# Kernel optimization log

Measured on AMD Instinct MI355X. Metric: run time of the kernel, lower is better.

## Reference

```python
import jax, jax.numpy as jnp
import numpy as np

V = 8000      # vocab size
D = 300       # node hidden size (GloVe-300)
B = 128       # documents per batch
L = 300       # max_length
NGRAM = 3     # window radius -> K = 2*NGRAM+1 neighbors (incl. self)
T = 2         # message-passing steps
E_NUM = 2_000_000  # edges_num (edge-weight embedding rows)
C = 54        # class_num


def setup_inputs() -> dict:
    key = jax.random.key(0)
    ks = jax.random.split(key, 6)
    docs = jax.random.randint(ks[0], (B, L), 0, V)                       # token ids per doc
    node_embed = jax.random.normal(ks[1], (V, D), jnp.float32) * 0.1     # node_hidden.weight
    node_eta = jax.random.uniform(ks[2], (V, 1), jnp.float32)            # node_eta.weight (rand init)
    edge_w = jax.random.uniform(ks[3], (E_NUM, 1), jnp.float32)          # seq_edge_w.weight (rand init)
    edges_matrix = jax.random.randint(ks[4], (V, V), 0, E_NUM, dtype=jnp.int32)  # word-pair -> edge id
    bn_gamma = jnp.ones((D,), jnp.float32)
    bn_beta = jnp.zeros((D,), jnp.float32)
    W = jax.random.normal(ks[5], (D, C), jnp.float32) * 0.05             # Linear weight
    b = jnp.zeros((C,), jnp.float32)
    return {"node_embed": node_embed, "node_eta": node_eta, "edge_w": edge_w,
            "bn_gamma": bn_gamma, "bn_beta": bn_beta, "W": W, "b": b,
            "docs": docs, "edges_matrix": edges_matrix}


def reference(node_embed, node_eta, edge_w, bn_gamma, bn_beta, W, b, docs, edges_matrix):
    B_, L_ = docs.shape
    # sliding-window graph (direction == 'both'): each position connects to +/-NGRAM positions
    offs = jnp.arange(-NGRAM, NGRAM + 1)                 # [K]
    nbr = jnp.arange(L_)[:, None] + offs[None, :]        # [L, K]
    valid = (nbr >= 0) & (nbr < L_)                      # mask edges off the doc ends
    nbrc = jnp.clip(nbr, 0, L_ - 1)

    src_words = docs[:, nbrc]                            # [B, L, K] neighbor token ids
    eids = edges_matrix[docs[:, :, None], src_words]     # [B, L, K] PMI edge-id gather
    w = edge_w[eids, 0]                                  # [B, L, K] edge weights

    h = node_embed[docs]                                 # [B, L, D] node features
    eta = node_eta[docs]                                 # [B, L, 1] per-word gate
    neg = jnp.finfo(h.dtype).min

    for _ in range(T):  # fixed small T: structural loop, not a data-dim loop
        nbr_h = h[:, nbrc, :]                            # [B, L, K, D]
        msg = jnp.max(jnp.where(valid[None, :, :, None], w[..., None] * nbr_h, neg), axis=2)
        h = eta * h + (1.0 - eta) * msg                  # gated update

    pooled = jnp.sum(h, axis=1)                          # [B, D] graph readout
    x = jax.nn.relu(pooled)
    mean = x.mean(axis=0)                                # BatchNorm1d (training-mode batch stats)
    var = x.var(axis=0)
    x = (x - mean) / jnp.sqrt(var + 1e-5) * bn_gamma + bn_beta
    return jax.nn.sigmoid(x @ W + b)                     # [B, C] multi-label probs
```

## Files before the change

kernel.cpp:

```cpp
#include <hip/hip_runtime.h>
#include <hip/hip_bf16.h>
#include <math.h>

#define V     8000
#define D_    300
#define B_    128
#define L_    300
#define C_    54
#define CHUNK 10
#define STR   11
#define NELEM (L_ * CHUNK)
#define KPT   12

__global__ __launch_bounds__(256) void wgather_kernel(
    const float* __restrict__ edge_w,
    const float* __restrict__ node_eta,
    const int*   __restrict__ docs,
    const int*   __restrict__ edges_matrix,
    float* __restrict__ w_ws,
    float* __restrict__ eta_ws)
{
    int idx = blockIdx.x * 256 + threadIdx.x;
    if (idx >= B_ * L_ * 7) return;
    int b   = idx / (L_ * 7);
    int rem = idx - b * (L_ * 7);
    int l   = rem / 7;
    int o   = rem - l * 7;
    const int* drow = docs + b * L_;
    int d1 = drow[l];
    int nb = min(max(l + o - 3, 0), L_ - 1);
    int d2 = drow[nb];
    int eid = edges_matrix[(size_t)d1 * V + d2];
    w_ws[((size_t)b * L_ + l) * 8 + o] = edge_w[eid];
    if (o == 3) eta_ws[b * L_ + l] = node_eta[d1];
}

__global__ __launch_bounds__(256, 4) void prop_kernel(
    const float* __restrict__ node_embed,
    const float* __restrict__ eta_ws,
    const float* __restrict__ w_ws,
    const int*   __restrict__ docs,
    float* __restrict__ pooled)
{
    int b   = blockIdx.y;
    int d0  = blockIdx.x * CHUNK;
    int tid = threadIdx.x;

    __shared__ float h_s[L_ * STR];
    __shared__ float w_s[L_ * 8];
    __shared__ float eta_s[L_];
    __shared__ int   docs_s[L_];
    __shared__ float red[25 * CHUNK];

    for (int l = tid; l < L_; l += 256) {
        docs_s[l] = docs[b * L_ + l];
        eta_s[l]  = eta_ws[b * L_ + l];
    }
    for (int i = tid; i < L_ * 8; i += 256)
        w_s[i] = w_ws[(size_t)b * (L_ * 8) + i];
    __syncthreads();

    #pragma unroll
    for (int k = 0; k < KPT; ++k) {
        int e = tid + k * 256;
        if (e < NELEM) {
            int l  = e / CHUNK;
            int dd = e - l * CHUNK;
            h_s[l * STR + dd] = node_embed[(size_t)docs_s[l] * D_ + d0 + dd];
        }
    }
    __syncthreads();

    for (int step = 0; step < 2; ++step) {
        float nv[KPT];
        #pragma unroll
        for (int k = 0; k < KPT; ++k) {
            int e = tid + k * 256;
            if (e < NELEM) {
                int l  = e / CHUNK;
                int dd = e - l * CHUNK;
                int a  = l * STR + dd;
                float own = h_s[a];
                float msg = -3.402823466e38f;
                #pragma unroll
                for (int o = 0; o < 7; ++o) {
                    int nb = l + o - 3;
                    if ((unsigned)nb < (unsigned)L_) {
                        float hv = (o == 3) ? own : h_s[a + (o - 3) * STR];
                        msg = fmaxf(msg, w_s[l * 8 + o] * hv);
                    }
                }
                float et = eta_s[l];
                nv[k] = et * own + (1.f - et) * msg;
            }
        }
        __syncthreads();
        #pragma unroll
        for (int k = 0; k < KPT; ++k) {
            int e = tid + k * 256;
            if (e < NELEM) {
                int l  = e / CHUNK;
                int dd = e - l * CHUNK;
                h_s[l * STR + dd] = nv[k];
            }
        }
        __syncthreads();
    }

    int grp = tid / CHUNK;
    int dd  = tid - grp * CHUNK;
    if (grp < 25) {
        float s = 0.f;
        #pragma unroll
        for (int j = 0; j < 12; ++j)
            s += h_s[(grp + j * 25) * STR + dd];
        red[grp * CHUNK + dd] = s;
    }
    __syncthreads();
    if (tid < CHUNK) {
        float s = 0.f;
        #pragma unroll
        for (int g = 0; g < 25; ++g) s += red[g * CHUNK + tid];
        pooled[b * D_ + d0 + tid] = s;
    }
}

__global__ __launch_bounds__(128) void bn_kernel(
    const float* __restrict__ pooled,
    const float* __restrict__ gamma,
    const float* __restrict__ beta,
    float* __restrict__ xn)
{
    int d = blockIdx.x;
    int b = threadIdx.x;
    float x = fmaxf(pooled[b * D_ + d], 0.f);

    float v1 = x, v2 = x * x;
    #pragma unroll
    for (int off = 32; off > 0; off >>= 1) {
        v1 += __shfl_down(v1, off, 64);
        v2 += __shfl_down(v2, off, 64);
    }
    __shared__ float s1[2], s2[2];
    int lane = b & 63, wv = b >> 6;
    if (lane == 0) { s1[wv] = v1; s2[wv] = v2; }
    __syncthreads();
    float mean = (s1[0] + s1[1]) * (1.f / 128.f);
    float var  = (s2[0] + s2[1]) * (1.f / 128.f) - mean * mean;
    float xh = (x - mean) / sqrtf(var + 1e-5f);
    xn[b * D_ + d] = xh * gamma[d] + beta[d];
}

__global__ __launch_bounds__(64) void out_kernel(
    const float* __restrict__ xn,
    const float* __restrict__ Wm,
    const float* __restrict__ bias,
    float* __restrict__ out)
{
    int b = blockIdx.x;
    int c = threadIdx.x;
    if (c >= C_) return;
    float acc = bias[c];
    for (int k = 0; k < D_; ++k)
        acc = fmaf(xn[b * D_ + k], Wm[k * C_ + c], acc);
    out[b * C_ + c] = 1.f / (1.f + expf(-acc));
}

extern "C" void kernel_launch(void* const* d_in, const int* in_sizes, int n_in,
                              void* d_out, int out_size, void* d_ws, size_t ws_size,
                              hipStream_t stream) {
    const float* node_embed   = (const float*)d_in[0];
    const float* node_eta     = (const float*)d_in[1];
    const float* edge_w       = (const float*)d_in[2];
    const float* bn_gamma     = (const float*)d_in[3];
    const float* bn_beta      = (const float*)d_in[4];
    const float* Wm           = (const float*)d_in[5];
    const float* bias         = (const float*)d_in[6];
    const int*   docs         = (const int*)d_in[7];
    const int*   edges_matrix = (const int*)d_in[8];
    float* out = (float*)d_out;

    float* w_ws   = (float*)d_ws;
    float* eta_ws = w_ws + (size_t)B_ * L_ * 8;
    float* pooled = eta_ws + (size_t)B_ * L_;
    float* xn     = pooled + (size_t)B_ * D_;

    {
        int total = B_ * L_ * 7;
        wgather_kernel<<<(total + 255) / 256, 256, 0, stream>>>(
            edge_w, node_eta, docs, edges_matrix, w_ws, eta_ws);
    }
    {
        dim3 grid(D_ / CHUNK, B_);
        prop_kernel<<<grid, 256, 0, stream>>>(node_embed, eta_ws, w_ws, docs, pooled);
    }
    bn_kernel<<<D_, 128, 0, stream>>>(pooled, bn_gamma, bn_beta, xn);
    out_kernel<<<B_, 64, 0, stream>>>(xn, Wm, bias, out);
}
```

Measured before the change: 381.6 us.

## Register-tile propagation with sliding windows, double-buffered LDS, and register-held weights

Each thread now owns one feature column over a run of 12 consecutive positions. It loads an 18-element sliding window from shared memory once per step instead of 7 reads per element, and keeps edge weights and eta in registers loaded with float4 reads. Ping-pong h buffers remove the extra barrier and writeback phase per step, and the docs/weights staging through shared memory is dropped. In exchange, register pressure rises sharply (about 96 weights plus a window), only 250 of 256 threads do work, and the occupancy hint in the launch bounds is removed.

After: 389.5 us. +2.1%, slower.

```diff
diff --git a/kernel.cpp b/kernel.cpp
--- a/kernel.cpp
+++ b/kernel.cpp
@@ -10,7 +10,8 @@
 #define CHUNK 10
 #define STR   11
 #define NELEM (L_ * CHUNK)
-#define KPT   12
+#define LRUN  12
+#define NGRP  25
 
 __global__ __launch_bounds__(256) void wgather_kernel(
     const float* __restrict__ edge_w,
@@ -35,7 +36,52 @@
     if (o == 3) eta_ws[b * L_ + l] = node_eta[d1];
 }
 
-__global__ __launch_bounds__(256, 4) void prop_kernel(
+__device__ __forceinline__ void prop_step(
+    const float* __restrict__ src, float* __restrict__ dst,
+    int l0, int dd, int lg, bool active,
+    const float w[LRUN][8], const float eta[LRUN])
+{
+    float win[18];
+    #pragma unroll
+    for (int i = 0; i < 18; ++i) {
+        int l = min(max(l0 - 3 + i, 0), L_ - 1);
+        win[i] = src[l * STR + dd];
+    }
+    if (active) {
+        if (lg > 0 && lg < NGRP - 1) {
+            #pragma unroll
+            for (int j = 0; j < LRUN; ++j) {
+                float own = win[j + 3];
+                float m = w[j][0] * win[j];
+                m = fmaxf(m, w[j][1] * win[j + 1]);
+                m = fmaxf(m, w[j][2] * win[j + 2]);
+                m = fmaxf(m, w[j][3] * own);
+                m = fmaxf(m, w[j][4] * win[j + 4]);
+                m = fmaxf(m, w[j][5] * win[j + 5]);
+                m = fmaxf(m, w[j][6] * win[j + 6]);
+                float et = eta[j];
+                dst[(l0 + j) * STR + dd] = et * own + (1.f - et) * m;
+            }
+        } else {
+            #pragma unroll
+            for (int j = 0; j < LRUN; ++j) {
+                int l = l0 + j;
+                float own = win[j + 3];
+                float m = -3.402823466e38f;
+                #pragma unroll
+                for (int o = 0; o < 7; ++o) {
+                    int nb = l - 3 + o;
+                    if (nb >= 0 && nb < L_)
+                        m = fmaxf(m, w[j][o] * win[j + o]);
+                }
+                float et = eta[j];
+                dst[l * STR + dd] = et * own + (1.f - et) * m;
+            }
+        }
+    }
+}
+
+__global__ __launch_bounds__(256) void prop_kernel(
     const float* __restrict__ node_embed,
     const float* __restrict__ eta_ws,
     const float* __restrict__ w_ws,
@@ -46,81 +92,67 @@
     int d0  = blockIdx.x * CHUNK;
     int tid = threadIdx.x;
 
-    __shared__ float h_s[L_ * STR];
-    __shared__ float w_s[L_ * 8];
-    __shared__ float eta_s[L_];
-    __shared__ int   docs_s[L_];
-    __shared__ float red[25 * CHUNK];
-
-    for (int l = tid; l < L_; l += 256) {
-        docs_s[l] = docs[b * L_ + l];
-        eta_s[l]  = eta_ws[b * L_ + l];
-    }
-    for (int i = tid; i < L_ * 8; i += 256)
-        w_s[i] = w_ws[(size_t)b * (L_ * 8) + i];
-    __syncthreads();
+    __shared__ float h_a[L_ * STR];
+    __shared__ float h_b[L_ * STR];
+    __shared__ float red[NGRP * CHUNK];
 
     #pragma unroll
-    for (int k = 0; k < KPT; ++k) {
+    for (int k = 0; k < 12; ++k) {
         int e = tid + k * 256;
         if (e < NELEM) {
             int l  = e / CHUNK;
             int dd = e - l * CHUNK;
-            h_s[l * STR + dd] = node_embed[(size_t)docs_s[l] * D_ + d0 + dd];
-        }
-    }
-    __syncthreads();
-
-    for (int step = 0; step < 2; ++step) {
-        float nv[KPT];
-        #pragma unroll
-        for (int k = 0; k < KPT; ++k) {
-            int e = tid + k * 256;
-            if (e < NELEM) {
-                int l  = e / CHUNK;
-                int dd = e - l * CHUNK;
-                int a  = l * STR + dd;
-                float own = h_s[a];
-                float msg = -3.402823466e38f;
-                #pragma unroll
-                for (int o = 0; o < 7; ++o) {
-                    int nb = l + o - 3;
-                    if ((unsigned)nb < (unsigned)L_) {
-                        float hv = (o == 3) ? own : h_s[a + (o - 3) * STR];
-                        msg = fmaxf(msg, w_s[l * 8 + o] * hv);
-                    }
-                }
-                float et = eta_s[l];
-                nv[k] = et * own + (1.f - et) * msg;
-            }
-        }
-        __syncthreads();
-        #pragma unroll
-        for (int k = 0; k < KPT; ++k) {
-            int e = tid + k * 256;
-            if (e < NELEM) {
-                int l  = e / CHUNK;
-                int dd = e - l * CHUNK;
-                h_s[l * STR + dd] = nv[k];
-            }
-        }
-        __syncthreads();
-    }
+            int row = docs[b * L_ + l];
+            h_a[l * STR + dd] = node_embed[(size_t)row * D_ + d0 + dd];
+        }
+    }
+
+    int dd = tid % CHUNK;
+    int lg = tid / CHUNK;
+    bool active = (tid < NGRP * CHUNK);
+    int lgc = min(lg, NGRP - 1);
+    int l0  = lgc * LRUN;
+
+    float w[LRUN][8];
+    float eta[LRUN];
+    {
+        const float4* wp = (const float4*)(w_ws + ((size_t)b * L_ + l0) * 8);
+        #pragma unroll
+        for (int j = 0; j < LRUN; ++j) {
+            float4 lo = wp[2 * j];
+            float4 hi = wp[2 * j + 1];
+            w[j][0] = lo.x; w[j][1] = lo.y; w[j][2] = lo.z; w[j][3] = lo.w;
+            w[j][4] = hi.x; w[j][5] = hi.y; w[j][6] = hi.z; w[j][7] = 0.f;
+        }
+        const float4* ep = (const float4*)(eta_ws + b * L_ + l0);
+        #pragma unroll
+        for (int j = 0; j < 3; ++j) {
+            float4 v = ep[j];
+            eta[4 * j + 0] = v.x; eta[4 * j + 1] = v.y;
+            eta[4 * j + 2] = v.z; eta[4 * j + 3] = v.w;
+        }
+    }
+    __syncthreads();
+
+    prop_step(h_a, h_b, l0, dd, lgc, active, w, eta);
+    __syncthreads();
+    prop_step(h_b, h_a, l0, dd, lgc, active, w, eta);
+    __syncthreads();
 
     int grp = tid / CHUNK;
-    int dd  = tid - grp * CHUNK;
-    if (grp < 25) {
+    int dd2 = tid - grp * CHUNK;
+    if (grp < NGRP) {
         float s = 0.f;
         #pragma unroll
         for (int j = 0; j < 12; ++j)
-            s += h_s[(grp + j * 25) * STR + dd];
-        red[grp * CHUNK + dd] = s;
+            s += h_a[(grp + j * NGRP) * STR + dd2];
+        red[grp * CHUNK + dd2] = s;
     }
     __syncthreads();
     if (tid < CHUNK) {
         float s = 0.f;
         #pragma unroll
-        for (int g = 0; g < 25; ++g) s += red[g * CHUNK + tid];
+        for (int g = 0; g < NGRP; ++g) s += red[g * CHUNK + tid];
         pooled[b * D_ + d0 + tid] = s;
     }
 }
```
